# Performance work log

Measured on AMD Instinct MI355X. Metric: run time of the kernel, lower is better.

The kernel has to match this reference:

```python
import jax, jax.numpy as jnp
import numpy as np

H = 512      # hidden_size = atom_fdim = mol_fdim
E = 4        # num_edge_types
DEPTH = 3    # args.depth
ATT_H = 128  # Attention hidden
NUM_ATOM_TYPES = 117


def setup_inputs() -> dict:
    key = jax.random.key(0)
    ks = jax.random.split(key, 24)
    N, A, F = 1024, 64, 1024
    s = 0.05
    nrm = lambda k, shape: jax.random.normal(k, shape, dtype=jnp.float32) * s
    inp = {}
    inp["atom_array"] = jax.random.randint(ks[0], (N, A), 0, NUM_ATOM_TYPES, dtype=jnp.int32)
    # sparse binary edge-typed molecular adjacency [N, E, A, A]
    inp["adj"] = (jax.random.uniform(ks[1], (N, E, A, A)) < 0.08).astype(jnp.float32)
    inp["features"] = jax.random.uniform(ks[2], (N, F), dtype=jnp.float32)
    # row-scaled dense stand-in for the normalized sparse drug-drug adjacency
    inp["adj_n"] = jax.random.uniform(ks[3], (N, N), dtype=jnp.float32) / N
    # --- GGNN params ---
    inp["embed_W"] = nrm(ks[4], (NUM_ATOM_TYPES, H))
    inp["msg_W"] = nrm(ks[5], (DEPTH, H, E * H))
    inp["msg_b"] = jnp.zeros((DEPTH, E * H), jnp.float32)
    inp["gru_Wih"] = nrm(ks[6], (H, 3 * H))
    inp["gru_Whh"] = nrm(ks[7], (H, 3 * H))
    inp["gru_bih"] = jnp.zeros((3 * H,), jnp.float32)
    inp["gru_bhh"] = jnp.zeros((3 * H,), jnp.float32)
    inp["i_W"] = nrm(ks[8], (2 * H, H)); inp["i_b"] = jnp.zeros((H,), jnp.float32)
    inp["j_W"] = nrm(ks[9], (H, H));     inp["j_b"] = jnp.zeros((H,), jnp.float32)
    # --- GCN params ---
    inp["gc_W1"] = nrm(ks[10], (F, H))
    inp["gc_W2"] = nrm(ks[11], (H, H))
    inp["gc_W3"] = nrm(ks[12], (H, H))
    inp["th_W"]  = nrm(ks[13], (H + F, H)); inp["th_b"]  = jnp.zeros((H,), jnp.float32)
    inp["th1_W"] = nrm(ks[14], (H + F, H)); inp["th1_b"] = jnp.zeros((H,), jnp.float32)
    inp["th2_W"] = nrm(ks[15], (H + F, H)); inp["th2_b"] = jnp.zeros((H,), jnp.float32)
    # --- Attention fusion ---
    inp["att_W1"] = nrm(ks[16], (H, ATT_H)); inp["att_b1"] = jnp.zeros((ATT_H,), jnp.float32)
    inp["att_W2"] = nrm(ks[17], (ATT_H, 1))
    return inp


def _gru_cell(m, h, Wih, Whh, bih, bhh):
    gi = m @ Wih + bih
    gh = h @ Whh + bhh
    ir, iz, inn = jnp.split(gi, 3, axis=-1)
    hr, hz, hn = jnp.split(gh, 3, axis=-1)
    r = jax.nn.sigmoid(ir + hr)
    z = jax.nn.sigmoid(iz + hz)
    n = jnp.tanh(inn + r * hn)
    return (1.0 - z) * n + z * h


def reference(atom_array, adj, features, adj_n, embed_W, msg_W, msg_b,
              gru_Wih, gru_Whh, gru_bih, gru_bhh, i_W, i_b, j_W, j_b,
              gc_W1, gc_W2, gc_W3, th_W, th_b, th1_W, th1_b, th2_W, th2_b,
              att_W1, att_b1, att_W2):
    N, A = atom_array.shape
    # ---- GGNN molecular encoder ----
    h0 = embed_W[atom_array]                     # [N, A, H]
    h = h0
    for step in range(DEPTH):
        m = (h @ msg_W[step] + msg_b[step]).reshape(N, A, E, H)   # [N, A, E, H]
        # edge-typed bmm + sum over edge types: adj[n,e,i,j] @ m[n,j,e,h]
        m = jnp.einsum('neij,njeh->nih', adj, m)                  # [N, A, H]
        hprev = h if step > 0 else jnp.zeros_like(h)              # GRUCell(h=None) -> zeros
        h = _gru_cell(m.reshape(N * A, H), hprev.reshape(N * A, H),
                      gru_Wih, gru_Whh, gru_bih, gru_bhh).reshape(N, A, H)
    # readout: gated sum/mean over atoms, averaged
    gate = jax.nn.sigmoid(jnp.concatenate([h, h0], axis=-1) @ i_W + i_b)
    ij = gate * (h @ j_W + j_b)                  # [N, A, H]
    g = (ij.mean(axis=1) + ij.sum(axis=1)) * 0.5  # [N, H]
    # ---- GCN drug encoder (dropout is identity in eval) ----
    gc = lambda x, W: adj_n @ (x @ W)            # spmm(adj, spmm(x, W))
    h1 = jax.nn.relu(jnp.concatenate([gc(features, gc_W1), features], axis=1) @ th_W + th_b)
    h2 = jax.nn.relu(jnp.concatenate([gc(h1, gc_W2), features], axis=1) @ th1_W + th1_b)
    emb = jax.nn.relu(jnp.concatenate([gc(h2, gc_W3), features], axis=1) @ th2_W + th2_b)
    # ---- attention fusion of the two views ----
    z = jnp.stack([g, emb], axis=1)              # [N, 2, H]
    w = jnp.tanh(z @ att_W1 + att_b1) @ att_W2   # [N, 2, 1]
    beta = jax.nn.softmax(w, axis=1)
    fused = (beta * z).sum(axis=1)               # [N, H]
    # ---- inner-product decoder ----
    rec = jax.nn.sigmoid(fused @ fused.T)        # [N, N]
    return rec
```

## Files before the change

kernel.cpp:

```cpp
#include <hip/hip_runtime.h>
#include <stdint.h>

#define DEV __device__ __forceinline__

#if defined(__has_builtin)
#if __has_builtin(__builtin_elementwise_fma)
#define HAVE_EW_FMA 1
#endif
#endif

typedef __attribute__((ext_vector_type(2))) float f32x2;

DEV float sigm(float x) { return 1.f / (1.f + __expf(-x)); }
DEV float tanh_fast(float x) {
    float e = __expf(-2.f * fabsf(x));
    float t = (1.f - e) / (1.f + e);
    return x < 0.f ? -t : t;
}

template<int ACT>
__global__ __launch_bounds__(256)
void k_fgemm(const float* __restrict__ A, int lda,
             const float* __restrict__ Bt, int ldb,
             const float* __restrict__ bias,
             float* __restrict__ C, int ldc, int K)
{
    __shared__ float As[16][132];
    __shared__ float Bs[16][132];
    const int t = threadIdx.x;
    const int tx = t & 15, ty = t >> 4;
    const long brow = (long)blockIdx.y * 128;
    const long bcol = (long)blockIdx.x * 128;
    const int sr = t >> 1;
    const int kq = (t & 1) * 8;

    f32x2 acc[8][4];
#pragma unroll
    for (int i = 0; i < 8; ++i)
#pragma unroll
        for (int j = 0; j < 4; ++j) acc[i][j] = (f32x2){0.f, 0.f};

    for (int kt = 0; kt < K; kt += 16) {
        const float4 a0 = *(const float4*)(A  + (brow + sr) * (long)lda + kt + kq);
        const float4 a1 = *(const float4*)(A  + (brow + sr) * (long)lda + kt + kq + 4);
        const float4 b0 = *(const float4*)(Bt + (bcol + sr) * (long)ldb + kt + kq);
        const float4 b1 = *(const float4*)(Bt + (bcol + sr) * (long)ldb + kt + kq + 4);
        As[kq + 0][sr] = a0.x; As[kq + 1][sr] = a0.y; As[kq + 2][sr] = a0.z; As[kq + 3][sr] = a0.w;
        As[kq + 4][sr] = a1.x; As[kq + 5][sr] = a1.y; As[kq + 6][sr] = a1.z; As[kq + 7][sr] = a1.w;
        Bs[kq + 0][sr] = b0.x; Bs[kq + 1][sr] = b0.y; Bs[kq + 2][sr] = b0.z; Bs[kq + 3][sr] = b0.w;
        Bs[kq + 4][sr] = b1.x; Bs[kq + 5][sr] = b1.y; Bs[kq + 6][sr] = b1.z; Bs[kq + 7][sr] = b1.w;
        __syncthreads();
#pragma unroll
        for (int kk = 0; kk < 16; ++kk) {
            float av[8], bv[8];
            *(float4*)&av[0] = *(const float4*)&As[kk][ty * 8];
            *(float4*)&av[4] = *(const float4*)&As[kk][ty * 8 + 4];
            *(float4*)&bv[0] = *(const float4*)&Bs[kk][tx * 8];
            *(float4*)&bv[4] = *(const float4*)&Bs[kk][tx * 8 + 4];
#pragma unroll
            for (int i = 0; i < 8; ++i) {
                const f32x2 ai = {av[i], av[i]};
#pragma unroll
                for (int j = 0; j < 4; ++j) {
                    const f32x2 bj = {bv[j * 2], bv[j * 2 + 1]};
#ifdef HAVE_EW_FMA
                    acc[i][j] = __builtin_elementwise_fma(ai, bj, acc[i][j]);
#else
                    acc[i][j].x = fmaf(ai.x, bj.x, acc[i][j].x);
                    acc[i][j].y = fmaf(ai.y, bj.y, acc[i][j].y);
#endif
                }
            }
        }
        __syncthreads();
    }

    float bb[8];
#pragma unroll
    for (int j = 0; j < 8; ++j) bb[j] = bias ? bias[bcol + tx * 8 + j] : 0.f;
#pragma unroll
    for (int i = 0; i < 8; ++i) {
        float o[8];
#pragma unroll
        for (int j = 0; j < 4; ++j) { o[j * 2] = acc[i][j].x + bb[j * 2]; o[j * 2 + 1] = acc[i][j].y + bb[j * 2 + 1]; }
#pragma unroll
        for (int j = 0; j < 8; ++j) {
            if (ACT == 1) o[j] = fmaxf(o[j], 0.f);
            if (ACT == 2) o[j] = sigm(o[j]);
        }
        float* cp = C + (brow + ty * 8 + i) * (long)ldc + bcol + tx * 8;
        *(float4*)cp = *(const float4*)&o[0];
        *(float4*)(cp + 4) = *(const float4*)&o[4];
    }
}

__global__ __launch_bounds__(256)
void k_transposeF(const float* __restrict__ W, float* __restrict__ Wt, int K, int N)
{
    __shared__ float tile[32][33];
    const int n0 = blockIdx.x * 32, k0 = blockIdx.y * 32;
    const int tx = threadIdx.x & 31, ty = threadIdx.x >> 5;
#pragma unroll
    for (int r = 0; r < 4; ++r)
        tile[ty + r * 8][tx] = W[(long)(k0 + ty + r * 8) * N + n0 + tx];
    __syncthreads();
#pragma unroll
    for (int r = 0; r < 4; ++r)
        Wt[(long)(n0 + ty + r * 8) * K + k0 + tx] = tile[tx][ty + r * 8];
}

__global__ void k_copyF(const float* __restrict__ s, float* __restrict__ d, int C, int ldd)
{
    const long idx = ((long)blockIdx.x * 256 + threadIdx.x) * 4;
    const long r = idx / C; const int c = (int)(idx % C);
    *(float4*)(d + r * (long)ldd + c) = *(const float4*)(s + r * (long)C + c);
}

__global__ void k_embedF(const int* __restrict__ at, const float* __restrict__ ew,
                         float* __restrict__ hcat)
{
    const long idx = (long)blockIdx.x * 256 + threadIdx.x;
    const long row = idx >> 6; const int c8 = (int)(idx & 63) * 8;
    const int tok = at[row];
    const float4 v0 = *(const float4*)(ew + (long)tok * 512 + c8);
    const float4 v1 = *(const float4*)(ew + (long)tok * 512 + c8 + 4);
    float* o = hcat + row * 1024 + c8;
    *(float4*)o = v0;           *(float4*)(o + 4) = v1;
    *(float4*)(o + 512) = v0;   *(float4*)(o + 516) = v1;
}

__global__ __launch_bounds__(256)
void k_einsum_s(const float* __restrict__ adj, const float* __restrict__ msg,
                float* __restrict__ mout)
{
    const int b = blockIdx.x;
    const int n = b >> 6, i = b & 63;
    const int t = threadIdx.x;
    float a0 = 0.f, a1 = 0.f;
#pragma unroll
    for (int e = 0; e < 4; ++e) {
        const float* ar = adj + (((long)n * 4 + e) * 64 + i) * 64;
        const float* me = msg + (long)n * 64 * 2048 + e * 512;
        for (int j = 0; j < 64; ++j) {
            if (ar[j] != 0.f) {
                const float* mr = me + (long)j * 2048;
                a0 += mr[t]; a1 += mr[t + 256];
            }
        }
    }
    mout[(long)b * 512 + t] = a0;
    mout[(long)b * 512 + t + 256] = a1;
}

template<int STEP0>
__global__ __launch_bounds__(256)
void k_gruF(const float* __restrict__ gi, const float* __restrict__ gh,
            const float* __restrict__ bhh, float* __restrict__ hcat)
{
    const long idx = (long)blockIdx.x * 256 + threadIdx.x;
    const long row = idx >> 7; const int c4 = (int)(idx & 127) * 4;
    const float* gir = gi + row * 1536 + c4;
    const float4 xr = *(const float4*)(gir);
    const float4 xz = *(const float4*)(gir + 512);
    const float4 xn = *(const float4*)(gir + 1024);
    float* hp = hcat + row * 1024 + c4;
    const float4 hv = *(const float4*)hp;
    float4 hr, hz, hn;
    if (STEP0) {
        hr = *(const float4*)(bhh + c4);
        hz = *(const float4*)(bhh + 512 + c4);
        hn = *(const float4*)(bhh + 1024 + c4);
    } else {
        const float* ghr = gh + row * 1536 + c4;
        hr = *(const float4*)(ghr);
        hz = *(const float4*)(ghr + 512);
        hn = *(const float4*)(ghr + 1024);
    }
    const float xra[4] = {xr.x, xr.y, xr.z, xr.w};
    const float xza[4] = {xz.x, xz.y, xz.z, xz.w};
    const float xna[4] = {xn.x, xn.y, xn.z, xn.w};
    const float hra[4] = {hr.x, hr.y, hr.z, hr.w};
    const float hza[4] = {hz.x, hz.y, hz.z, hz.w};
    const float hna[4] = {hn.x, hn.y, hn.z, hn.w};
    const float hva[4] = {hv.x, hv.y, hv.z, hv.w};
    float o[4];
#pragma unroll
    for (int k = 0; k < 4; ++k) {
        const float hprev = STEP0 ? 0.f : hva[k];
        const float r = sigm(xra[k] + hra[k]);
        const float z = sigm(xza[k] + hza[k]);
        const float nn = tanh_fast(xna[k] + r * hna[k]);
        o[k] = (1.f - z) * nn + z * hprev;
    }
    float4 ov; ov.x = o[0]; ov.y = o[1]; ov.z = o[2]; ov.w = o[3];
    *(float4*)hp = ov;
}

__global__ __launch_bounds__(256)
void k_readout(const float* __restrict__ gate, const float* __restrict__ jj, float* __restrict__ g)
{
    const int n = blockIdx.x, t = threadIdx.x;
    float a0 = 0.f, a1 = 0.f;
    for (int a = 0; a < 64; ++a) {
        const long base = ((long)n * 64 + a) * 512;
        a0 += gate[base + t] * jj[base + t];
        a1 += gate[base + t + 256] * jj[base + t + 256];
    }
    g[(long)n * 512 + t]       = a0 * (65.f / 128.f);
    g[(long)n * 512 + t + 256] = a1 * (65.f / 128.f);
}

__global__ __launch_bounds__(128)
void k_att(const float* __restrict__ g, const float* __restrict__ emb,
           const float* __restrict__ W1, const float* __restrict__ bias1,
           const float* __restrict__ W2, float* __restrict__ fused)
{
    __shared__ float v[512];
    __shared__ float red[128];
    __shared__ float sres[2];
    const int n = blockIdx.x, t = threadIdx.x;
    for (int view = 0; view < 2; ++view) {
        const float* src = (view ? emb : g) + (long)n * 512;
        for (int k = t; k < 512; k += 128) v[k] = src[k];
        __syncthreads();
        float acc = bias1[t];
        for (int k = 0; k < 512; ++k) acc += v[k] * W1[k * 128 + t];
        red[t] = tanh_fast(acc) * W2[t];
        __syncthreads();
        if (t == 0) { float s = 0.f; for (int i = 0; i < 128; ++i) s += red[i]; sres[view] = s; }
        __syncthreads();
    }
    const float b0 = 1.f / (1.f + __expf(sres[1] - sres[0]));
    const float b1v = 1.f - b0;
    for (int k = t; k < 512; k += 128) {
        fused[(long)n * 512 + k] = b0 * g[(long)n * 512 + k] + b1v * emb[(long)n * 512 + k];
    }
}

static void sgemm(hipStream_t st, const float* A, int lda, const float* B, int ldb,
                  const float* bias, float* C, int ldc, int M, int N, int K, int act)
{
    dim3 g(N / 128, M / 128), b(256);
    if (act == 0)      k_fgemm<0><<<g, b, 0, st>>>(A, lda, B, ldb, bias, C, ldc, K);
    else if (act == 1) k_fgemm<1><<<g, b, 0, st>>>(A, lda, B, ldb, bias, C, ldc, K);
    else               k_fgemm<2><<<g, b, 0, st>>>(A, lda, B, ldb, bias, C, ldc, K);
}

extern "C" void kernel_launch(void* const* d_in, const int* in_sizes, int n_in,
                              void* d_out, int out_size, void* d_ws, size_t ws_size,
                              hipStream_t stream)
{
    const int*   atom = (const int*)  d_in[0];
    const float* adj  = (const float*)d_in[1];
    const float* feat = (const float*)d_in[2];
    const float* adjn = (const float*)d_in[3];
    const float* embW = (const float*)d_in[4];
    const float* msgW = (const float*)d_in[5];
    const float* msgb = (const float*)d_in[6];
    const float* Wih  = (const float*)d_in[7];
    const float* Whh  = (const float*)d_in[8];
    const float* bih  = (const float*)d_in[9];
    const float* bhh  = (const float*)d_in[10];
    const float* iW   = (const float*)d_in[11];
    const float* ib   = (const float*)d_in[12];
    const float* jW   = (const float*)d_in[13];
    const float* jb   = (const float*)d_in[14];
    const float* gc1  = (const float*)d_in[15];
    const float* gc2  = (const float*)d_in[16];
    const float* gc3  = (const float*)d_in[17];
    const float* thW  = (const float*)d_in[18];
    const float* thb  = (const float*)d_in[19];
    const float* th1W = (const float*)d_in[20];
    const float* th1b = (const float*)d_in[21];
    const float* th2W = (const float*)d_in[22];
    const float* th2b = (const float*)d_in[23];
    const float* aW1  = (const float*)d_in[24];
    const float* ab1  = (const float*)d_in[25];
    const float* aW2  = (const float*)d_in[26];

    constexpr size_t O_WTMSG = 0;
    constexpr size_t O_WTWIH = O_WTMSG + (size_t)3 * 2048 * 512 * 4;
    constexpr size_t O_WTWHH = O_WTWIH + (size_t)1536 * 512 * 4;
    constexpr size_t O_WTIW  = O_WTWHH + (size_t)1536 * 512 * 4;
    constexpr size_t O_WTJW  = O_WTIW  + (size_t)512 * 1024 * 4;
    constexpr size_t O_WTGC1 = O_WTJW  + (size_t)512 * 512 * 4;
    constexpr size_t O_WTGC2 = O_WTGC1 + (size_t)512 * 1024 * 4;
    constexpr size_t O_WTGC3 = O_WTGC2 + (size_t)512 * 512 * 4;
    constexpr size_t O_WTTH  = O_WTGC3 + (size_t)512 * 512 * 4;
    constexpr size_t O_WTTH1 = O_WTTH  + (size_t)512 * 1536 * 4;
    constexpr size_t O_WTTH2 = O_WTTH1 + (size_t)512 * 1536 * 4;
    constexpr size_t O_GCAT  = O_WTTH2 + (size_t)512 * 1536 * 4;
    constexpr size_t O_PT    = O_GCAT  + (size_t)1024 * 1536 * 4;
    constexpr size_t O_H1    = O_PT    + (size_t)512 * 1024 * 4;
    constexpr size_t O_H2    = O_H1    + (size_t)1024 * 512 * 4;
    constexpr size_t O_EMBF  = O_H2    + (size_t)1024 * 512 * 4;
    constexpr size_t O_GF    = O_EMBF  + (size_t)1024 * 512 * 4;
    constexpr size_t O_FUSED = O_GF    + (size_t)1024 * 512 * 4;
    constexpr size_t O_CHUNK = O_FUSED + (size_t)1024 * 512 * 4;

    int C = 1024;
    while (C > 2 && O_CHUNK + (size_t)64 * C * 20480 > ws_size) C >>= 1;
    if (O_CHUNK + (size_t)64 * C * 20480 > ws_size) return;
    const int R = C * 64;
    const int nchunks = 1024 / C;

    uint8_t* wsb = (uint8_t*)d_ws;
    float* wtMsg = (float*)(wsb + O_WTMSG);
    float* wtWih = (float*)(wsb + O_WTWIH);
    float* wtWhh = (float*)(wsb + O_WTWHH);
    float* wtIw  = (float*)(wsb + O_WTIW);
    float* wtJw  = (float*)(wsb + O_WTJW);
    float* wtGc1 = (float*)(wsb + O_WTGC1);
    float* wtGc2 = (float*)(wsb + O_WTGC2);
    float* wtGc3 = (float*)(wsb + O_WTGC3);
    float* wtTh  = (float*)(wsb + O_WTTH);
    float* wtTh1 = (float*)(wsb + O_WTTH1);
    float* wtTh2 = (float*)(wsb + O_WTTH2);
    float* gcatF = (float*)(wsb + O_GCAT);
    float* ptF   = (float*)(wsb + O_PT);
    float* h1F   = (float*)(wsb + O_H1);
    float* h2F   = (float*)(wsb + O_H2);
    float* embF  = (float*)(wsb + O_EMBF);
    float* gF    = (float*)(wsb + O_GF);
    float* fusedF= (float*)(wsb + O_FUSED);
    uint8_t* cr = wsb + O_CHUNK;
    float* hcatF = (float*)(cr);
    float* ghF   = (float*)(cr + (size_t)R * 4096);
    float* maggF = (float*)(cr + (size_t)R * 10240);
    float* msgF  = (float*)(cr + (size_t)R * 12288);
    float* giF   = msgF;
    float* gateF = msgF;
    float* jjF   = msgF + (size_t)R * 512;

    for (int s = 0; s < 3; ++s)
        k_transposeF<<<dim3(64, 16), 256, 0, stream>>>(msgW + (size_t)s * 512 * 2048,
                                                       wtMsg + (size_t)s * 2048 * 512, 512, 2048);
    k_transposeF<<<dim3(48, 16), 256, 0, stream>>>(Wih, wtWih, 512, 1536);
    k_transposeF<<<dim3(48, 16), 256, 0, stream>>>(Whh, wtWhh, 512, 1536);
    k_transposeF<<<dim3(16, 32), 256, 0, stream>>>(iW,  wtIw, 1024, 512);
    k_transposeF<<<dim3(16, 16), 256, 0, stream>>>(jW,  wtJw,  512, 512);
    k_transposeF<<<dim3(16, 32), 256, 0, stream>>>(gc1, wtGc1, 1024, 512);
    k_transposeF<<<dim3(16, 16), 256, 0, stream>>>(gc2, wtGc2, 512, 512);
    k_transposeF<<<dim3(16, 16), 256, 0, stream>>>(gc3, wtGc3, 512, 512);
    k_transposeF<<<dim3(16, 48), 256, 0, stream>>>(thW,  wtTh,  1536, 512);
    k_transposeF<<<dim3(16, 48), 256, 0, stream>>>(th1W, wtTh1, 1536, 512);
    k_transposeF<<<dim3(16, 48), 256, 0, stream>>>(th2W, wtTh2, 1536, 512);
    k_copyF<<<1024, 256, 0, stream>>>(feat, gcatF + 512, 1024, 1536);

    for (int c = 0; c < nchunks; ++c) {
        const size_t arow0 = (size_t)c * R;
        k_embedF<<<R / 4, 256, 0, stream>>>(atom + arow0, embW, hcatF);
        for (int s = 0; s < 3; ++s) {
            sgemm(stream, hcatF, 1024, wtMsg + (size_t)s * 2048 * 512, 512,
                  msgb + (size_t)s * 2048, msgF, 2048, R, 2048, 512, 0);
            k_einsum_s<<<R, 256, 0, stream>>>(adj + (size_t)c * C * 4 * 64 * 64, msgF, maggF);
            sgemm(stream, maggF, 512, wtWih, 512, bih, giF, 1536, R, 1536, 512, 0);
            if (s > 0)
                sgemm(stream, hcatF, 1024, wtWhh, 512, bhh, ghF, 1536, R, 1536, 512, 0);
            if (s == 0) k_gruF<1><<<R / 2, 256, 0, stream>>>(giF, nullptr, bhh, hcatF);
            else        k_gruF<0><<<R / 2, 256, 0, stream>>>(giF, ghF, bhh, hcatF);
        }
        sgemm(stream, hcatF, 1024, wtIw, 1024, ib, gateF, 512, R, 512, 1024, 2);
        sgemm(stream, hcatF, 1024, wtJw,  512, jb, jjF,   512, R, 512,  512, 0);
        k_readout<<<C, 256, 0, stream>>>(gateF, jjF, gF + (size_t)c * C * 512);
    }

    sgemm(stream, wtGc1, 1024, feat, 1024, nullptr, ptF, 1024, 512, 1024, 1024, 0);
    sgemm(stream, adjn, 1024, ptF, 1024, nullptr, gcatF, 1536, 1024, 512, 1024, 0);
    sgemm(stream, gcatF, 1536, wtTh, 1536, thb, h1F, 512, 1024, 512, 1536, 1);
    sgemm(stream, wtGc2, 512, h1F, 512, nullptr, ptF, 1024, 512, 1024, 512, 0);
    sgemm(stream, adjn, 1024, ptF, 1024, nullptr, gcatF, 1536, 1024, 512, 1024, 0);
    sgemm(stream, gcatF, 1536, wtTh1, 1536, th1b, h2F, 512, 1024, 512, 1536, 1);
    sgemm(stream, wtGc3, 512, h2F, 512, nullptr, ptF, 1024, 512, 1024, 512, 0);
    sgemm(stream, adjn, 1024, ptF, 1024, nullptr, gcatF, 1536, 1024, 512, 1024, 0);
    sgemm(stream, gcatF, 1536, wtTh2, 1536, th2b, embF, 512, 1024, 512, 1536, 1);

    k_att<<<1024, 128, 0, stream>>>(gF, embF, aW1, ab1, aW2, fusedF);
    sgemm(stream, fusedF, 512, fusedF, 512, nullptr, (float*)d_out, 1024, 1024, 1024, 512, 2);
}
```

Measured before the change: 17.25 ms.

## Double-buffer shared tiles and split B columns in fp32 GEMM kernel

Adds double-buffered shared memory so the next K-slab's global loads are issued before the current slab's FMAs, which also drops one barrier per iteration. Replaces packed f32x2 FMAs with scalar fmaf. Remaps each thread's 8 output columns into two groups of 4 spaced 64 apart, meant to reduce LDS bank conflicts on B reads and give better-coalesced stores. The cost is twice the LDS per block and more live registers for the prefetched values, which may lower occupancy. Losing the packed FMA could also reduce arithmetic throughput if the compiler was emitting v_pk_fma.

```diff
diff --git a/kernel.cpp b/kernel.cpp
--- a/kernel.cpp
+++ b/kernel.cpp
@@ -2,14 +2,6 @@
 #include <stdint.h>
 
 #define DEV __device__ __forceinline__
-
-#if defined(__has_builtin)
-#if __has_builtin(__builtin_elementwise_fma)
-#define HAVE_EW_FMA 1
-#endif
-#endif
-
-typedef __attribute__((ext_vector_type(2))) float f32x2;
 
 DEV float sigm(float x) { return 1.f / (1.f + __expf(-x)); }
 DEV float tanh_fast(float x) {
@@ -25,8 +17,8 @@
              const float* __restrict__ bias,
              float* __restrict__ C, int ldc, int K)
 {
-    __shared__ float As[16][132];
-    __shared__ float Bs[16][132];
+    __shared__ float As[2][16][132];
+    __shared__ float Bs[2][16][132];
     const int t = threadIdx.x;
     const int tx = t & 15, ty = t >> 4;
     const long brow = (long)blockIdx.y * 128;
@@ -34,63 +26,79 @@
     const int sr = t >> 1;
     const int kq = (t & 1) * 8;
 
-    f32x2 acc[8][4];
+    float acc[8][8];
 #pragma unroll
     for (int i = 0; i < 8; ++i)
 #pragma unroll
-        for (int j = 0; j < 4; ++j) acc[i][j] = (f32x2){0.f, 0.f};
-
-    for (int kt = 0; kt < K; kt += 16) {
-        const float4 a0 = *(const float4*)(A  + (brow + sr) * (long)lda + kt + kq);
-        const float4 a1 = *(const float4*)(A  + (brow + sr) * (long)lda + kt + kq + 4);
-        const float4 b0 = *(const float4*)(Bt + (bcol + sr) * (long)ldb + kt + kq);
-        const float4 b1 = *(const float4*)(Bt + (bcol + sr) * (long)ldb + kt + kq + 4);
-        As[kq + 0][sr] = a0.x; As[kq + 1][sr] = a0.y; As[kq + 2][sr] = a0.z; As[kq + 3][sr] = a0.w;
-        As[kq + 4][sr] = a1.x; As[kq + 5][sr] = a1.y; As[kq + 6][sr] = a1.z; As[kq + 7][sr] = a1.w;
-        Bs[kq + 0][sr] = b0.x; Bs[kq + 1][sr] = b0.y; Bs[kq + 2][sr] = b0.z; Bs[kq + 3][sr] = b0.w;
-        Bs[kq + 4][sr] = b1.x; Bs[kq + 5][sr] = b1.y; Bs[kq + 6][sr] = b1.z; Bs[kq + 7][sr] = b1.w;
-        __syncthreads();
+        for (int j = 0; j < 8; ++j) acc[i][j] = 0.f;
+
+    const float* pa = A + (brow + sr) * (long)lda + kq;
+    const float* pb = Bt + (bcol + sr) * (long)ldb + kq;
+
+    {
+        const float4 a0 = *(const float4*)(pa);
+        const float4 a1 = *(const float4*)(pa + 4);
+        const float4 b0 = *(const float4*)(pb);
+        const float4 b1 = *(const float4*)(pb + 4);
+        As[0][kq + 0][sr] = a0.x; As[0][kq + 1][sr] = a0.y; As[0][kq + 2][sr] = a0.z; As[0][kq + 3][sr] = a0.w;
+        As[0][kq + 4][sr] = a1.x; As[0][kq + 5][sr] = a1.y; As[0][kq + 6][sr] = a1.z; As[0][kq + 7][sr] = a1.w;
+        Bs[0][kq + 0][sr] = b0.x; Bs[0][kq + 1][sr] = b0.y; Bs[0][kq + 2][sr] = b0.z; Bs[0][kq + 3][sr] = b0.w;
+        Bs[0][kq + 4][sr] = b1.x; Bs[0][kq + 5][sr] = b1.y; Bs[0][kq + 6][sr] = b1.z; Bs[0][kq + 7][sr] = b1.w;
+    }
+    __syncthreads();
+
+    const int nslab = K >> 4;
+    for (int it = 0; it < nslab; ++it) {
+        const int cur = it & 1, nxt = cur ^ 1;
+        float4 na0, na1, nb0, nb1;
+        const bool more = (it + 1) < nslab;
+        if (more) {
+            const float* qa = pa + (it + 1) * 16;
+            const float* qb = pb + (it + 1) * 16;
+            na0 = *(const float4*)(qa);
+            na1 = *(const float4*)(qa + 4);
+            nb0 = *(const float4*)(qb);
+            nb1 = *(const float4*)(qb + 4);
+        }
 #pragma unroll
         for (int kk = 0; kk < 16; ++kk) {
             float av[8], bv[8];
-            *(float4*)&av[0] = *(const float4*)&As[kk][ty * 8];
-            *(float4*)&av[4] = *(const float4*)&As[kk][ty * 8 + 4];
-            *(float4*)&bv[0] = *(const float4*)&Bs[kk][tx * 8];
-            *(float4*)&bv[4] = *(const float4*)&Bs[kk][tx * 8 + 4];
-#pragma unroll
-            for (int i = 0; i < 8; ++i) {
-                const f32x2 ai = {av[i], av[i]};
-#pragma unroll
-                for (int j = 0; j < 4; ++j) {
-                    const f32x2 bj = {bv[j * 2], bv[j * 2 + 1]};
-#ifdef HAVE_EW_FMA
-                    acc[i][j] = __builtin_elementwise_fma(ai, bj, acc[i][j]);
-#else
-                    acc[i][j].x = fmaf(ai.x, bj.x, acc[i][j].x);
-                    acc[i][j].y = fmaf(ai.y, bj.y, acc[i][j].y);
-#endif
-                }
-            }
+            *(float4*)&av[0] = *(const float4*)&As[cur][kk][ty * 8];
+            *(float4*)&av[4] = *(const float4*)&As[cur][kk][ty * 8 + 4];
+            *(float4*)&bv[0] = *(const float4*)&Bs[cur][kk][tx * 4];
+            *(float4*)&bv[4] = *(const float4*)&Bs[cur][kk][tx * 4 + 64];
+#pragma unroll
+            for (int i = 0; i < 8; ++i)
+#pragma unroll
+                for (int j = 0; j < 8; ++j)
+                    acc[i][j] = fmaf(av[i], bv[j], acc[i][j]);
+        }
+        if (more) {
+            As[nxt][kq + 0][sr] = na0.x; As[nxt][kq + 1][sr] = na0.y; As[nxt][kq + 2][sr] = na0.z; As[nxt][kq + 3][sr] = na0.w;
+            As[nxt][kq + 4][sr] = na1.x; As[nxt][kq + 5][sr] = na1.y; As[nxt][kq + 6][sr] = na1.z; As[nxt][kq + 7][sr] = na1.w;
+            Bs[nxt][kq + 0][sr] = nb0.x; Bs[nxt][kq + 1][sr] = nb0.y; Bs[nxt][kq + 2][sr] = nb0.z; Bs[nxt][kq + 3][sr] = nb0.w;
+            Bs[nxt][kq + 4][sr] = nb1.x; Bs[nxt][kq + 5][sr] = nb1.y; Bs[nxt][kq + 6][sr] = nb1.z; Bs[nxt][kq + 7][sr] = nb1.w;
         }
         __syncthreads();
     }
 
     float bb[8];
 #pragma unroll
-    for (int j = 0; j < 8; ++j) bb[j] = bias ? bias[bcol + tx * 8 + j] : 0.f;
+    for (int j = 0; j < 8; ++j)
+        bb[j] = bias ? bias[bcol + tx * 4 + (j >> 2) * 64 + (j & 3)] : 0.f;
 #pragma unroll
     for (int i = 0; i < 8; ++i) {
         float o[8];
 #pragma unroll
-        for (int j = 0; j < 4; ++j) { o[j * 2] = acc[i][j].x + bb[j * 2]; o[j * 2 + 1] = acc[i][j].y + bb[j * 2 + 1]; }
-#pragma unroll
         for (int j = 0; j < 8; ++j) {
-            if (ACT == 1) o[j] = fmaxf(o[j], 0.f);
-            if (ACT == 2) o[j] = sigm(o[j]);
-        }
-        float* cp = C + (brow + ty * 8 + i) * (long)ldc + bcol + tx * 8;
+            float v = acc[i][j] + bb[j];
+            if (ACT == 1) v = fmaxf(v, 0.f);
+            if (ACT == 2) v = sigm(v);
+            o[j] = v;
+        }
+        float* cp = C + (brow + ty * 8 + i) * (long)ldc + bcol + tx * 4;
         *(float4*)cp = *(const float4*)&o[0];
-        *(float4*)(cp + 4) = *(const float4*)&o[4];
+        *(float4*)(cp + 64) = *(const float4*)&o[4];
     }
 }
 
```

After: 23.23 ms. 1.35x slower.
